# Optimization experiments

Measured on AMD Instinct MI355X. Metric: run time of the kernel, lower is better.

The kernel has to match this reference:

```python
import jax, jax.numpy as jnp
import numpy as np

B, L, D_ENC = 32, 512, 512
STEPS = 32
E_DIM = 128      # embedding_dim
A_DIM = 256      # attention_dim
H = 512          # hidden_size
VOCAB = 32000


def _linear(x, W, b):
    return x @ W.T + b


def setup_inputs() -> dict:
    key = jax.random.key(0)
    ks = jax.random.split(key, 12)
    s = lambda fan_in: 1.0 / np.sqrt(fan_in)
    return {
        "encoder_outputs": jax.random.normal(ks[0], (B, L, D_ENC), dtype=jnp.float32),
        "target_seq": jax.random.randint(ks[1], (B, STEPS), 0, VOCAB, dtype=jnp.int64),
        "pos_embedding": jax.random.normal(ks[2], (STEPS, E_DIM), dtype=jnp.float32),
        "dec_proj_W": jax.random.uniform(ks[3], (A_DIM, E_DIM), minval=-s(E_DIM), maxval=s(E_DIM)),
        "dec_proj_b": jnp.zeros((A_DIM,), jnp.float32),
        "enc_proj_W": jax.random.uniform(ks[4], (A_DIM, D_ENC), minval=-s(D_ENC), maxval=s(D_ENC)),
        "enc_proj_b": jnp.zeros((A_DIM,), jnp.float32),
        "attn_score_W": jax.random.uniform(ks[5], (1, A_DIM), minval=-s(A_DIM), maxval=s(A_DIM)),
        "attn_score_b": jnp.zeros((1,), jnp.float32),
        "hidden_proj_W": jax.random.uniform(ks[6], (H, E_DIM), minval=-s(E_DIM), maxval=s(E_DIM)),
        "hidden_proj_b": jnp.zeros((H,), jnp.float32),
        "fc_out_W": jax.random.uniform(ks[7], (VOCAB, H + D_ENC), minval=-s(H + D_ENC), maxval=s(H + D_ENC)),
        "fc_out_b": jnp.zeros((VOCAB,), jnp.float32),
    }


def reference(encoder_outputs, target_seq, pos_embedding,
              dec_proj_W, dec_proj_b, enc_proj_W, enc_proj_b,
              attn_score_W, attn_score_b, hidden_proj_W, hidden_proj_b,
              fc_out_W, fc_out_b):
    batch = encoder_outputs.shape[0]
    steps = target_seq.shape[1]
    # [B, L, A]
    enc_proj = _linear(encoder_outputs, enc_proj_W, enc_proj_b)
    # [B, S, E]  (dropout=0 in eval)
    pos_emb = jnp.broadcast_to(pos_embedding[:steps][None], (batch, steps, pos_embedding.shape[1]))
    # [B, S, A]
    dec_query = _linear(pos_emb, dec_proj_W, dec_proj_b)
    # additive attention: [B, S, L, A]
    combined = jnp.tanh(enc_proj[:, None, :, :] + dec_query[:, :, None, :])
    # score reduction to scalar: [B, S, L]
    attn_scores = jnp.einsum('bsla,a->bsl', combined, attn_score_W[0]) + attn_score_b[0]
    attn_weights = jax.nn.softmax(attn_scores, axis=2)
    # context: [B, S, D_enc]
    context = jnp.einsum('bsl,bld->bsd', attn_weights, encoder_outputs)
    hidden = _linear(pos_emb, hidden_proj_W, hidden_proj_b)  # [B, S, H]
    logits = _linear(jnp.concatenate([hidden, context], axis=-1), fc_out_W, fc_out_b)
    return logits
```

## Files before the change

kernel.cpp:

```cpp
#include <hip/hip_runtime.h>
#include <hip/hip_bf16.h>
#include <stdint.h>

typedef __attribute__((ext_vector_type(4))) float f32x4;
typedef __attribute__((ext_vector_type(8))) short short8;

#define B_   32
#define L_   512
#define DE_  512
#define S_   32
#define ED_  128
#define AD_  256
#define HD_  512
#define VOC_ 32000
#define M_   1024

__device__ __forceinline__ unsigned short f2bf(float f){
  union { float f; unsigned int u; } v; v.f = f;
  unsigned int u = v.u;
  unsigned int r = (u + 0x7FFFu + ((u >> 16) & 1u)) >> 16;
  return (unsigned short)r;
}

__device__ __forceinline__ float bf2f(unsigned short u){
  union { unsigned int u; float f; } v; v.u = ((unsigned int)u) << 16;
  return v.f;
}

__device__ __forceinline__ float tanh_fast(float x){
  float t = __expf(2.0f * x);
  return (t - 1.0f) * __builtin_amdgcn_rcpf(t + 1.0f);
}

__device__ __forceinline__ void gl_lds16(const void* g, void* l){
  __builtin_amdgcn_global_load_lds(
      (const __attribute__((address_space(1))) unsigned int*)g,
      (__attribute__((address_space(3))) unsigned int*)l, 16, 0, 0);
}

extern "C" __global__ void __launch_bounds__(256)
k_cvt(const float* __restrict__ src, unsigned short* __restrict__ dst, int n4){
  int stride = gridDim.x * 256;
  for (int i = blockIdx.x * 256 + threadIdx.x; i < n4; i += stride){
    f32x4 v = ((const f32x4*)src)[i];
    ushort4 o;
    o.x = f2bf(v[0]); o.y = f2bf(v[1]); o.z = f2bf(v[2]); o.w = f2bf(v[3]);
    ((ushort4*)dst)[i] = o;
  }
}

extern "C" __global__ void __launch_bounds__(256)
k_cvtW(const float* __restrict__ fcW, unsigned short* __restrict__ Wc, int n4){
  int stride = gridDim.x * 256;
  for (int i = blockIdx.x * 256 + threadIdx.x; i < n4; i += stride){
    int row = i >> 7;
    int c4  = i & 127;
    f32x4 v = *(const f32x4*)&fcW[(size_t)row * 1024 + 512 + c4 * 4];
    ushort4 o;
    o.x = f2bf(v[0]); o.y = f2bf(v[1]); o.z = f2bf(v[2]); o.w = f2bf(v[3]);
    *(ushort4*)&Wc[(size_t)row * 512 + c4 * 4] = o;
  }
}

extern "C" __global__ void __launch_bounds__(256)
k_small(const float* __restrict__ pos, const float* __restrict__ dW, const float* __restrict__ db,
        const float* __restrict__ hW, const float* __restrict__ hb,
        float* __restrict__ dq, unsigned short* __restrict__ hbf){
  int t = blockIdx.x * 256 + threadIdx.x;
  if (t < S_ * AD_){
    int s = t >> 8, a = t & 255;
    const float* p = pos + s * ED_;
    const float* wrow = dW + a * ED_;
    float acc = db[a];
    #pragma unroll 4
    for (int e = 0; e < ED_; ++e) acc += p[e] * wrow[e];
    dq[t] = acc;
  } else if (t < S_ * AD_ + S_ * HD_){
    int u = t - S_ * AD_;
    int s = u >> 9, h = u & 511;
    const float* p = pos + s * ED_;
    const float* wrow = hW + h * ED_;
    float acc = hb[h];
    #pragma unroll 4
    for (int e = 0; e < ED_; ++e) acc += p[e] * wrow[e];
    hbf[u] = f2bf(acc);
  }
}

extern "C" __global__ void __launch_bounds__(256)
k_gemm_encp(const unsigned short* __restrict__ A, const unsigned short* __restrict__ Bt,
            const float* __restrict__ bias, unsigned short* __restrict__ C){
  __shared__ unsigned short As[128 * 32];
  __shared__ unsigned short Bs[128 * 32];
  int bm = blockIdx.x >> 1, bn = blockIdx.x & 1;
  int tid = threadIdx.x, wid = tid >> 6, lane = tid & 63;
  int fr = lane & 15, fq = lane >> 4;
  int wm = wid >> 1, wn = wid & 1;
  f32x4 acc[4][4];
  #pragma unroll
  for (int i = 0; i < 4; ++i)
    #pragma unroll
    for (int j = 0; j < 4; ++j) acc[i][j] = (f32x4)0.0f;

  for (int k0 = 0; k0 < 512; k0 += 32){
    __syncthreads();
    #pragma unroll
    for (int i = 0; i < 2; ++i){
      int seg = wid * 2 + i;
      int row = seg * 16 + (lane >> 2);
      int col = (lane & 3) * 8;
      gl_lds16(A  + (size_t)(bm * 128 + row) * 512 + k0 + col, &As[seg * 512]);
      gl_lds16(Bt + (size_t)(bn * 128 + row) * 512 + k0 + col, &Bs[seg * 512]);
    }
    __syncthreads();
    short8 a[4], b[4];
    #pragma unroll
    for (int mf = 0; mf < 4; ++mf) a[mf] = *(const short8*)&As[(wm * 64 + mf * 16 + fr) * 32 + fq * 8];
    #pragma unroll
    for (int nf = 0; nf < 4; ++nf) b[nf] = *(const short8*)&Bs[(wn * 64 + nf * 16 + fr) * 32 + fq * 8];
    #pragma unroll
    for (int mf = 0; mf < 4; ++mf)
      #pragma unroll
      for (int nf = 0; nf < 4; ++nf)
        acc[mf][nf] = __builtin_amdgcn_mfma_f32_16x16x32_bf16(a[mf], b[nf], acc[mf][nf], 0, 0, 0);
  }
  #pragma unroll
  for (int mf = 0; mf < 4; ++mf){
    int row = bm * 128 + wm * 64 + mf * 16 + fq * 4;
    #pragma unroll
    for (int nf = 0; nf < 4; ++nf){
      int col = bn * 128 + wn * 64 + nf * 16 + fr;
      float bv = bias[col];
      #pragma unroll
      for (int j = 0; j < 4; ++j)
        C[(size_t)(row + j) * 256 + col] = f2bf(acc[mf][nf][j] + bv);
    }
  }
}

extern "C" __global__ void __launch_bounds__(256)
k_attn(const unsigned short* __restrict__ encp, const float* __restrict__ dq,
       const float* __restrict__ vW, float* __restrict__ wgt){
  int idx = blockIdx.x;
  int wg = (idx & 7) * 128 + (idx >> 3);
  int b = wg >> 5, s = wg & 31;
  int tid = threadIdx.x, wid = tid >> 6, lane = tid & 63;
  int half = lane >> 5, a0 = (lane & 31) * 8;
  __shared__ float sc[512];
  __shared__ float redm[4], reds[4];
  f32x4 dqa = *(const f32x4*)&dq[s * AD_ + a0];
  f32x4 dqb = *(const f32x4*)&dq[s * AD_ + a0 + 4];
  f32x4 va  = *(const f32x4*)&vW[a0];
  f32x4 vb  = *(const f32x4*)&vW[a0 + 4];
  for (int it = 0; it < 64; ++it){
    int l = wid * 128 + it * 2 + half;
    short8 e8 = *(const short8*)&encp[((size_t)(b * 512 + l)) * 256 + a0];
    float p = 0.0f;
    #pragma unroll
    for (int j = 0; j < 4; ++j) p += tanh_fast(bf2f((unsigned short)e8[j]) + dqa[j]) * va[j];
    #pragma unroll
    for (int j = 0; j < 4; ++j) p += tanh_fast(bf2f((unsigned short)e8[4 + j]) + dqb[j]) * vb[j];
    #pragma unroll
    for (int off = 16; off >= 1; off >>= 1) p += __shfl_xor(p, off);
    if ((lane & 31) == 0) sc[l] = p;
  }
  __syncthreads();
  float s0 = sc[tid], s1 = sc[tid + 256];
  float m = fmaxf(s0, s1);
  #pragma unroll
  for (int off = 32; off >= 1; off >>= 1) m = fmaxf(m, __shfl_xor(m, off));
  if (lane == 0) redm[wid] = m;
  __syncthreads();
  m = fmaxf(fmaxf(redm[0], redm[1]), fmaxf(redm[2], redm[3]));
  float e0 = __expf(s0 - m), e1 = __expf(s1 - m);
  float sum = e0 + e1;
  #pragma unroll
  for (int off = 32; off >= 1; off >>= 1) sum += __shfl_xor(sum, off);
  if (lane == 0) reds[wid] = sum;
  __syncthreads();
  float tot = reds[0] + reds[1] + reds[2] + reds[3];
  float inv = __builtin_amdgcn_rcpf(tot);
  size_t base = (size_t)(b * 32 + s) * 512;
  wgt[base + tid] = e0 * inv;
  wgt[base + tid + 256] = e1 * inv;
}

extern "C" __global__ void __launch_bounds__(256)
k_ctx(const float* __restrict__ enc, const float* __restrict__ wgt, unsigned short* __restrict__ ctx){
  int b = blockIdx.x >> 4, dt = blockIdx.x & 15;
  int tid = threadIdx.x;
  __shared__ float wl[32 * 512];
  #pragma unroll 8
  for (int i = 0; i < 64; ++i)
    wl[i * 256 + tid] = wgt[(size_t)b * 16384 + i * 256 + tid];
  __syncthreads();
  int d = dt * 32 + (tid & 31);
  int grp = tid >> 5;
  float acc0 = 0, acc1 = 0, acc2 = 0, acc3 = 0;
  const float* ebase = enc + (size_t)b * 262144 + d;
  const float* w0 = &wl[(grp * 4 + 0) * 512];
  const float* w1 = &wl[(grp * 4 + 1) * 512];
  const float* w2 = &wl[(grp * 4 + 2) * 512];
  const float* w3 = &wl[(grp * 4 + 3) * 512];
  #pragma unroll 8
  for (int l = 0; l < 512; ++l){
    float e = ebase[(size_t)l * 512];
    acc0 += w0[l] * e; acc1 += w1[l] * e; acc2 += w2[l] * e; acc3 += w3[l] * e;
  }
  size_t obase = (size_t)(b * 32 + grp * 4) * 512 + d;
  ctx[obase]        = f2bf(acc0);
  ctx[obase + 512]  = f2bf(acc1);
  ctx[obase + 1024] = f2bf(acc2);
  ctx[obase + 1536] = f2bf(acc3);
}

extern "C" __global__ void __launch_bounds__(256)
k_logh(const unsigned short* __restrict__ hbf, const float* __restrict__ fcW,
       const float* __restrict__ fcb, float* __restrict__ logh){
  int bn = blockIdx.x;
  int tid = threadIdx.x, wid = tid >> 6, lane = tid & 63;
  int fr = lane & 15, fq = lane >> 4;
  int col = bn * 64 + wid * 16 + fr;
  const float* brow = fcW + (size_t)col * 1024;
  f32x4 acc0 = (f32x4)0.0f, acc1 = (f32x4)0.0f;
  #pragma unroll 4
  for (int k0 = 0; k0 < 512; k0 += 32){
    int ko = k0 + fq * 8;
    f32x4 b0 = *(const f32x4*)(brow + ko);
    f32x4 b1 = *(const f32x4*)(brow + ko + 4);
    short8 bfr;
    bfr[0] = (short)f2bf(b0[0]); bfr[1] = (short)f2bf(b0[1]);
    bfr[2] = (short)f2bf(b0[2]); bfr[3] = (short)f2bf(b0[3]);
    bfr[4] = (short)f2bf(b1[0]); bfr[5] = (short)f2bf(b1[1]);
    bfr[6] = (short)f2bf(b1[2]); bfr[7] = (short)f2bf(b1[3]);
    short8 a0 = *(const short8*)&hbf[(size_t)fr * 512 + ko];
    short8 a1 = *(const short8*)&hbf[(size_t)(16 + fr) * 512 + ko];
    acc0 = __builtin_amdgcn_mfma_f32_16x16x32_bf16(a0, bfr, acc0, 0, 0, 0);
    acc1 = __builtin_amdgcn_mfma_f32_16x16x32_bf16(a1, bfr, acc1, 0, 0, 0);
  }
  float bv = fcb[col];
  #pragma unroll
  for (int j = 0; j < 4; ++j){
    logh[(size_t)(fq * 4 + j) * VOC_ + col]      = acc0[j] + bv;
    logh[(size_t)(16 + fq * 4 + j) * VOC_ + col] = acc1[j] + bv;
  }
}

extern "C" __global__ void __launch_bounds__(256)
k_gemm_main(const unsigned short* __restrict__ Abf, const unsigned short* __restrict__ Wc,
            const float* __restrict__ logh, float* __restrict__ out){
  __shared__ unsigned short As[128 * 32];
  __shared__ unsigned short Bs[128 * 32];
  int idx = blockIdx.x;
  int wg = (idx & 7) * 250 + (idx >> 3);
  int bm = wg & 7, bn = wg >> 3;
  int tid = threadIdx.x, wid = tid >> 6, lane = tid & 63;
  int fr = lane & 15, fq = lane >> 4;
  int wm = wid >> 1, wn = wid & 1;
  f32x4 acc[4][4];
  #pragma unroll
  for (int i = 0; i < 4; ++i)
    #pragma unroll
    for (int j = 0; j < 4; ++j) acc[i][j] = (f32x4)0.0f;

  for (int k0 = 0; k0 < 512; k0 += 32){
    __syncthreads();
    #pragma unroll
    for (int i = 0; i < 2; ++i){
      int seg = wid * 2 + i;
      int row = seg * 16 + (lane >> 2);
      int col = (lane & 3) * 8;
      gl_lds16(Abf + (size_t)(bm * 128 + row) * 512 + k0 + col, &As[seg * 512]);
      gl_lds16(Wc  + (size_t)(bn * 128 + row) * 512 + k0 + col, &Bs[seg * 512]);
    }
    __syncthreads();
    short8 a[4], b[4];
    #pragma unroll
    for (int mf = 0; mf < 4; ++mf) a[mf] = *(const short8*)&As[(wm * 64 + mf * 16 + fr) * 32 + fq * 8];
    #pragma unroll
    for (int nf = 0; nf < 4; ++nf) b[nf] = *(const short8*)&Bs[(wn * 64 + nf * 16 + fr) * 32 + fq * 8];
    #pragma unroll
    for (int mf = 0; mf < 4; ++mf)
      #pragma unroll
      for (int nf = 0; nf < 4; ++nf)
        acc[mf][nf] = __builtin_amdgcn_mfma_f32_16x16x32_bf16(a[mf], b[nf], acc[mf][nf], 0, 0, 0);
  }
  #pragma unroll
  for (int mf = 0; mf < 4; ++mf){
    int rowb = bm * 128 + wm * 64 + mf * 16 + fq * 4;
    #pragma unroll
    for (int nf = 0; nf < 4; ++nf){
      int col = bn * 128 + wn * 64 + nf * 16 + fr;
      #pragma unroll
      for (int j = 0; j < 4; ++j){
        int r = rowb + j;
        out[(size_t)r * VOC_ + col] = acc[mf][nf][j] + logh[(size_t)(r & 31) * VOC_ + col];
      }
    }
  }
}

extern "C" void kernel_launch(void* const* d_in, const int* in_sizes, int n_in,
                              void* d_out, int out_size, void* d_ws, size_t ws_size,
                              hipStream_t stream){
  const float* enc = (const float*)d_in[0];
  const float* pos = (const float*)d_in[2];
  const float* dW  = (const float*)d_in[3];
  const float* db  = (const float*)d_in[4];
  const float* eW  = (const float*)d_in[5];
  const float* eb  = (const float*)d_in[6];
  const float* vW  = (const float*)d_in[7];
  const float* hW  = (const float*)d_in[9];
  const float* hb  = (const float*)d_in[10];
  const float* fcW = (const float*)d_in[11];
  const float* fcb = (const float*)d_in[12];
  float* out = (float*)d_out;

  char* w = (char*)d_ws;
  unsigned short* Wc_bf   = (unsigned short*)(w);
  unsigned short* enc_bf  = (unsigned short*)(w + 32768000);
  unsigned short* encp_bf = (unsigned short*)(w + 49545216);
  unsigned short* ctx     = (unsigned short*)(w + 57933824);
  float*          logh    = (float*)(w + 58982400);
  float*          dq      = (float*)(w + 63078400);
  unsigned short* hbf     = (unsigned short*)(w + 63111168);
  unsigned short* encW_bf = (unsigned short*)(w + 63143936);
  float*          wgt     = (float*)(w + 63406080);

  k_cvt<<<dim3(2048), dim3(256), 0, stream>>>(enc, enc_bf, 8388608 / 4);
  k_cvt<<<dim3(128), dim3(256), 0, stream>>>(eW, encW_bf, 131072 / 4);
  k_cvtW<<<dim3(2048), dim3(256), 0, stream>>>(fcW, Wc_bf, 32000 * 512 / 4);
  k_small<<<dim3(96), dim3(256), 0, stream>>>(pos, dW, db, hW, hb, dq, hbf);
  k_gemm_encp<<<dim3(256), dim3(256), 0, stream>>>(enc_bf, encW_bf, eb, encp_bf);
  k_attn<<<dim3(1024), dim3(256), 0, stream>>>(encp_bf, dq, vW, wgt);
  k_ctx<<<dim3(512), dim3(256), 0, stream>>>(enc, wgt, ctx);
  k_logh<<<dim3(500), dim3(256), 0, stream>>>(hbf, fcW, fcb, logh);
  k_gemm_main<<<dim3(2000), dim3(256), 0, stream>>>(ctx, Wc_bf, logh, out);
}
```

Measured before the change: 229.7 us.

## Enlarge main GEMM tile to 256x256 with double-buffered LDS and XCD remap

Measured after the change: 231.1 us. About the same (+0.6%).

```diff
diff --git a/kernel.cpp b/kernel.cpp
--- a/kernel.cpp
+++ b/kernel.cpp
@@ -246,55 +246,72 @@
   }
 }
 
-extern "C" __global__ void __launch_bounds__(256)
+extern "C" __global__ void __launch_bounds__(512, 2)
 k_gemm_main(const unsigned short* __restrict__ Abf, const unsigned short* __restrict__ Wc,
             const float* __restrict__ logh, float* __restrict__ out){
-  __shared__ unsigned short As[128 * 32];
-  __shared__ unsigned short Bs[128 * 32];
-  int idx = blockIdx.x;
-  int wg = (idx & 7) * 250 + (idx >> 3);
-  int bm = wg & 7, bn = wg >> 3;
+  __shared__ unsigned short As[2][256 * 32];
+  __shared__ unsigned short Bs[2][256 * 32];
+  int orig = blockIdx.x;
+  int xcd = orig & 7, j = orig >> 3;
+  int wgid = (xcd < 4 ? xcd * 63 : 252 + (xcd - 4) * 62) + j;
+  int bm = wgid & 3, bn = wgid >> 2;
   int tid = threadIdx.x, wid = tid >> 6, lane = tid & 63;
   int fr = lane & 15, fq = lane >> 4;
-  int wm = wid >> 1, wn = wid & 1;
-  f32x4 acc[4][4];
-  #pragma unroll
-  for (int i = 0; i < 4; ++i)
-    #pragma unroll
-    for (int j = 0; j < 4; ++j) acc[i][j] = (f32x4)0.0f;
-
-  for (int k0 = 0; k0 < 512; k0 += 32){
-    __syncthreads();
-    #pragma unroll
-    for (int i = 0; i < 2; ++i){
-      int seg = wid * 2 + i;
-      int row = seg * 16 + (lane >> 2);
-      int col = (lane & 3) * 8;
-      gl_lds16(Abf + (size_t)(bm * 128 + row) * 512 + k0 + col, &As[seg * 512]);
-      gl_lds16(Wc  + (size_t)(bn * 128 + row) * 512 + k0 + col, &Bs[seg * 512]);
+  int wm = wid >> 2, wn = wid & 3;
+  int abase = bm * 256, bbase = bn * 256;
+  int srow = (lane >> 2), scol = (lane & 3) * 8;
+
+  f32x4 acc[8][4];
+  #pragma unroll
+  for (int i = 0; i < 8; ++i)
+    #pragma unroll
+    for (int jj = 0; jj < 4; ++jj) acc[i][jj] = (f32x4)0.0f;
+
+  {
+    int c0 = wid * 2;
+    gl_lds16(Abf + (size_t)(abase + c0 * 16 + srow) * 512 + scol,        &As[0][c0 * 512]);
+    gl_lds16(Abf + (size_t)(abase + c0 * 16 + 16 + srow) * 512 + scol,   &As[0][c0 * 512 + 512]);
+    gl_lds16(Wc  + (size_t)(bbase + c0 * 16 + srow) * 512 + scol,        &Bs[0][c0 * 512]);
+    gl_lds16(Wc  + (size_t)(bbase + c0 * 16 + 16 + srow) * 512 + scol,   &Bs[0][c0 * 512 + 512]);
+  }
+  __syncthreads();
+
+  int cur = 0;
+  for (int t = 0; t < 16; ++t){
+    if (t < 15){
+      int k0n = (t + 1) * 32;
+      int c0 = wid * 2;
+      gl_lds16(Abf + (size_t)(abase + c0 * 16 + srow) * 512 + k0n + scol,      &As[cur ^ 1][c0 * 512]);
+      gl_lds16(Abf + (size_t)(abase + c0 * 16 + 16 + srow) * 512 + k0n + scol, &As[cur ^ 1][c0 * 512 + 512]);
+      gl_lds16(Wc  + (size_t)(bbase + c0 * 16 + srow) * 512 + k0n + scol,      &Bs[cur ^ 1][c0 * 512]);
+      gl_lds16(Wc  + (size_t)(bbase + c0 * 16 + 16 + srow) * 512 + k0n + scol, &Bs[cur ^ 1][c0 * 512 + 512]);
     }
-    __syncthreads();
-    short8 a[4], b[4];
-    #pragma unroll
-    for (int mf = 0; mf < 4; ++mf) a[mf] = *(const short8*)&As[(wm * 64 + mf * 16 + fr) * 32 + fq * 8];
-    #pragma unroll
-    for (int nf = 0; nf < 4; ++nf) b[nf] = *(const short8*)&Bs[(wn * 64 + nf * 16 + fr) * 32 + fq * 8];
-    #pragma unroll
-    for (int mf = 0; mf < 4; ++mf)
+    short8 a[8], b[4];
+    #pragma unroll
+    for (int mf = 0; mf < 8; ++mf)
+      a[mf] = *(const short8*)&As[cur][(wm * 128 + mf * 16 + fr) * 32 + fq * 8];
+    #pragma unroll
+    for (int nf = 0; nf < 4; ++nf)
+      b[nf] = *(const short8*)&Bs[cur][(wn * 64 + nf * 16 + fr) * 32 + fq * 8];
+    #pragma unroll
+    for (int mf = 0; mf < 8; ++mf)
       #pragma unroll
       for (int nf = 0; nf < 4; ++nf)
         acc[mf][nf] = __builtin_amdgcn_mfma_f32_16x16x32_bf16(a[mf], b[nf], acc[mf][nf], 0, 0, 0);
-  }
-  #pragma unroll
-  for (int mf = 0; mf < 4; ++mf){
-    int rowb = bm * 128 + wm * 64 + mf * 16 + fq * 4;
+    __syncthreads();
+    cur ^= 1;
+  }
+
+  #pragma unroll
+  for (int mf = 0; mf < 8; ++mf){
+    int rowb = bm * 256 + wm * 128 + mf * 16 + fq * 4;
     #pragma unroll
     for (int nf = 0; nf < 4; ++nf){
-      int col = bn * 128 + wn * 64 + nf * 16 + fr;
+      int col = bn * 256 + wn * 64 + nf * 16 + fr;
       #pragma unroll
-      for (int j = 0; j < 4; ++j){
-        int r = rowb + j;
-        out[(size_t)r * VOC_ + col] = acc[mf][nf][j] + logh[(size_t)(r & 31) * VOC_ + col];
+      for (int jj = 0; jj < 4; ++jj){
+        int r = rowb + jj;
+        out[(size_t)r * VOC_ + col] = acc[mf][nf][jj] + logh[(size_t)(r & 31) * VOC_ + col];
       }
     }
   }
@@ -335,5 +352,5 @@
   k_attn<<<dim3(1024), dim3(256), 0, stream>>>(encp_bf, dq, vW, wgt);
   k_ctx<<<dim3(512), dim3(256), 0, stream>>>(enc, wgt, ctx);
   k_logh<<<dim3(500), dim3(256), 0, stream>>>(hbf, fcW, fcb, logh);
-  k_gemm_main<<<dim3(2000), dim3(256), 0, stream>>>(ctx, Wc_bf, logh, out);
-}
+  k_gemm_main<<<dim3(500), dim3(512), 0, stream>>>(ctx, Wc_bf, logh, out);
+}
```
